# Kernel optimization log

Measured on AMD Instinct MI355X. Metric: run time of the kernel, lower is better.

The kernel has to match this reference:

```python
import jax, jax.numpy as jnp
import numpy as np

B, T, I, H = 64, 512, 1024, 1024

def setup_inputs() -> dict:
    key = jax.random.key(0)
    k1, k2, k3, k4, k5 = jax.random.split(key, 5)
    s_x = 1.0 / np.sqrt(I)
    s_h = 1.0 / np.sqrt(H)
    return {
        "x": jax.random.normal(k1, (B, T, I), dtype=jnp.float32),
        "Wx": jax.random.uniform(k2, (I, H), minval=-s_x, maxval=s_x, dtype=jnp.float32),
        "bx": jax.random.uniform(k3, (H,), minval=-s_x, maxval=s_x, dtype=jnp.float32),
        "Wh": jax.random.uniform(k4, (H, H), minval=-s_h, maxval=s_h, dtype=jnp.float32),
        "bh": jax.random.uniform(k5, (H,), minval=-s_h, maxval=s_h, dtype=jnp.float32),
    }

def reference(x, Wx, bx, Wh, bh):
    # Precompute input projections for all timesteps in one big GEMM: [B,T,H]
    xproj = jnp.einsum("bti,ih->bth", x, Wx) + bx + bh
    h0 = jnp.zeros((x.shape[0], Wh.shape[0]), dtype=x.dtype)

    def step(h, xp_t):
        h_new = jnp.tanh(xp_t + h @ Wh)
        return h_new, h_new

    # scan over time: xproj transposed to [T,B,H]
    h_last, outs = jax.lax.scan(step, h0, jnp.swapaxes(xproj, 0, 1))
    return jnp.swapaxes(outs, 0, 1), h_last
```

## Files before the change

kernel.cpp:

```cpp
#include <hip/hip_runtime.h>


#define Bdim 64
#define Tdim 512
#define Idim 1024
#define Hdim 1024
#define Mdim (Bdim * Tdim)

typedef __attribute__((ext_vector_type(8))) short bf16x8;
typedef __attribute__((ext_vector_type(4))) float f32x4;
typedef __attribute__((ext_vector_type(4))) unsigned int u32x4;

__device__ __forceinline__ float tanh_fast(float x) {
  float e = __expf(2.0f * x);
  return 1.0f - 2.0f / (e + 1.0f);
}
__device__ __forceinline__ unsigned int f2bf(float f) {
  unsigned int u = __float_as_uint(f);
  return (u + 0x7FFFu + ((u >> 16) & 1u)) >> 16;
}
__device__ __forceinline__ unsigned int pack2(float lo, float hi) {
  return f2bf(lo) | (f2bf(hi) << 16);
}

__global__ __launch_bounds__(256) void cvt_transpose(
    const float* __restrict__ src, unsigned short* __restrict__ dst) {
  __shared__ float t[32][33];
  const int bx = blockIdx.x * 32;
  const int by = blockIdx.y * 32;
  const int ty = threadIdx.x >> 3;
  const int tx = threadIdx.x & 7;
  float4 v = *(const float4*)&src[(size_t)(by + ty) * 1024 + bx + tx * 4];
  t[ty][tx * 4 + 0] = v.x; t[ty][tx * 4 + 1] = v.y;
  t[ty][tx * 4 + 2] = v.z; t[ty][tx * 4 + 3] = v.w;
  __syncthreads();
  ushort4 o;
  o.x = (unsigned short)f2bf(t[tx * 4 + 0][ty]);
  o.y = (unsigned short)f2bf(t[tx * 4 + 1][ty]);
  o.z = (unsigned short)f2bf(t[tx * 4 + 2][ty]);
  o.w = (unsigned short)f2bf(t[tx * 4 + 3][ty]);
  *(ushort4*)&dst[(size_t)(bx + ty) * 1024 + by + tx * 4] = o;
}

__global__ __launch_bounds__(256) void xg_mfma(
    const float* __restrict__ X,
    const unsigned short* __restrict__ WxT,
    const float* __restrict__ bx, const float* __restrict__ bh,
    float* __restrict__ C) {
  __shared__ char sAB[16384] __attribute__((aligned(16)));
  char* sA = sAB;
  char* sB = sAB + 8192;
  const int tid = threadIdx.x;
  const int m0 = blockIdx.y * 128;
  const int n0 = blockIdx.x * 128;
  const int w = tid >> 6, l = tid & 63;
  const int wm = (w >> 1) * 64, wn = (w & 1) * 64;
  const int r2 = tid >> 1, kh = tid & 1;

  f32x4 acc[4][4];
#pragma unroll
  for (int i = 0; i < 4; ++i)
#pragma unroll
    for (int j = 0; j < 4; ++j) acc[i][j] = (f32x4){0.f, 0.f, 0.f, 0.f};

  for (int k0 = 0; k0 < Idim; k0 += 32) {
    const float* xa = &X[(size_t)(m0 + r2) * Idim + k0 + kh * 16];
    float4 a0 = *(const float4*)(xa + 0), a1 = *(const float4*)(xa + 4);
    float4 a2 = *(const float4*)(xa + 8), a3 = *(const float4*)(xa + 12);
    const char* wb = (const char*)&WxT[(size_t)(n0 + r2) * Idim + k0 + kh * 16];
    u32x4 b0 = *(const u32x4*)wb;
    u32x4 b1 = *(const u32x4*)(wb + 16);
    __syncthreads();
    u32x4 pa0 = {pack2(a0.x, a0.y), pack2(a0.z, a0.w),
                 pack2(a1.x, a1.y), pack2(a1.z, a1.w)};
    u32x4 pa1 = {pack2(a2.x, a2.y), pack2(a2.z, a2.w),
                 pack2(a3.x, a3.y), pack2(a3.z, a3.w)};
    const int sw = (r2 & 7) << 4;
    const int rb = r2 * 64 + kh * 32;
    *(u32x4*)(sA + ((rb + 0) ^ sw)) = pa0;
    *(u32x4*)(sA + ((rb + 16) ^ sw)) = pa1;
    *(u32x4*)(sB + ((rb + 0) ^ sw)) = b0;
    *(u32x4*)(sB + ((rb + 16) ^ sw)) = b1;
    __syncthreads();
    bf16x8 af[4], bf[4];
#pragma unroll
    for (int i = 0; i < 4; ++i) {
      int ra = wm + i * 16 + (l & 15);
      af[i] = *(const bf16x8*)(sA + ((ra * 64 + (l >> 4) * 16) ^ ((ra & 7) << 4)));
      int rn = wn + i * 16 + (l & 15);
      bf[i] = *(const bf16x8*)(sB + ((rn * 64 + (l >> 4) * 16) ^ ((rn & 7) << 4)));
    }
#pragma unroll
    for (int i = 0; i < 4; ++i)
#pragma unroll
      for (int j = 0; j < 4; ++j)
        acc[i][j] = __builtin_amdgcn_mfma_f32_16x16x32_bf16(af[i], bf[j],
                                                            acc[i][j], 0, 0, 0);
  }
  float bias[4];
#pragma unroll
  for (int j = 0; j < 4; ++j) {
    int c = n0 + wn + j * 16 + (l & 15);
    bias[j] = bx[c] + bh[c];
  }
#pragma unroll
  for (int i = 0; i < 4; ++i) {
    int rbase = m0 + wm + i * 16 + (l >> 4) * 4;
#pragma unroll
    for (int j = 0; j < 4; ++j) {
      int c = n0 + wn + j * 16 + (l & 15);
#pragma unroll
      for (int r = 0; r < 4; ++r)
        C[(size_t)(rbase + r) * Hdim + c] = acc[i][j][r] + bias[j];
    }
  }
}

__global__ __launch_bounds__(512, 2) void rnn_scan(
    const unsigned short* __restrict__ WhT,
    float* __restrict__ out,
    float* __restrict__ hlast,
    unsigned long long* hbuf) {
  const int bid = blockIdx.x;
  const int cl = bid & 3;
  const int cg = bid >> 2;
  const int tid = threadIdx.x;
  const int w = tid >> 6;
  const int l = tid & 63;
  const int n0 = cg * 64;

  __shared__ char smem[32768 + 33280] __attribute__((aligned(16)));
  char* smh = smem;
  char* smp = smem + 32768;

  bf16x8 bfrag[16];
  {
    const int col = n0 + (l & 15);
    const int kb = (w << 7) + ((l >> 4) << 3);
#pragma unroll
    for (int nt = 0; nt < 4; ++nt)
#pragma unroll
      for (int kt = 0; kt < 4; ++kt)
        bfrag[nt * 4 + kt] =
            *(const bf16x8*)&WhT[(size_t)(col + nt * 16) * 1024 + kb + kt * 32];
  }

  const int fb = tid >> 5;
  const int jj = tid & 31;
  const int c0 = 2 * jj;
  const int b_abs = cl * 16 + fb;
  const int nt0 = c0 >> 4;
  const int lane0 = ((fb >> 2) << 4) | (c0 & 15);
  const int reg4 = (fb & 3) * 4;
  const size_t obase = ((size_t)b_abs * Tdim) * Hdim + n0 + c0;

  float2 xp = *(const float2*)&out[obase];

  for (int t = 0; t < Tdim; ++t) {
    float sum0 = 0.f, sum1 = 0.f;
    if (t > 0) {
      const int arow = l & 15;
      const int ab = arow * 2048 + (w << 8) + ((l >> 4) << 4);
      const int sw = (arow & 7) << 4;
      bf16x8 af[4];
#pragma unroll
      for (int kt = 0; kt < 4; ++kt)
        af[kt] = *(const bf16x8*)(smh + ((ab + kt * 64) ^ sw));
#pragma unroll
      for (int nt = 0; nt < 4; ++nt) {
        f32x4 a = {0.f, 0.f, 0.f, 0.f};
#pragma unroll
        for (int kt = 0; kt < 4; ++kt)
          a = __builtin_amdgcn_mfma_f32_16x16x32_bf16(af[kt], bfrag[nt * 4 + kt],
                                                      a, 0, 0, 0);
        *(f32x4*)(smp + (((w * 4 + nt) * 65 + l) << 4)) = a;
      }
      __syncthreads();
#pragma unroll
      for (int w8 = 0; w8 < 8; ++w8) {
        const char* p0 = smp + (((w8 * 4 + nt0) * 65 + lane0) << 4) + reg4;
        sum0 += *(const float*)p0;
        sum1 += *(const float*)(p0 + 16);
      }
    }
    float h0 = tanh_fast(xp.x + sum0);
    float h1 = tanh_fast(xp.y + sum1);
    if (t == Tdim - 1) {
      *(float2*)&out[obase + (size_t)t * Hdim] = make_float2(h0, h1);
      *(float2*)&hlast[(size_t)b_abs * Hdim + n0 + c0] = make_float2(h0, h1);
      break;
    }
    const int par = (t + 1) & 1;
    unsigned long long pv =
        ((unsigned long long)(unsigned int)(t + 1) << 32) |
        (unsigned long long)pack2(h0, h1);
    __hip_atomic_store(&hbuf[(size_t)par * 32768 + (size_t)b_abs * 512 +
                             (n0 >> 1) + jj],
                       pv, __ATOMIC_RELAXED, __HIP_MEMORY_SCOPE_AGENT);
    *(float2*)&out[obase + (size_t)t * Hdim] = make_float2(h0, h1);
    xp = *(const float2*)&out[obase + (size_t)(t + 1) * Hdim];
    {
      const char* src =
          (const char*)hbuf + (size_t)par * 262144 + (size_t)cl * 65536;
      u32x4 v[8];
      const unsigned int tgt = (unsigned int)(t + 1);
      for (;;) {
#pragma unroll
        for (int i = 0; i < 8; ++i) {
          const char* p = src + ((size_t)(tid + i * 512) << 4);
          asm volatile("global_load_dwordx4 %0, %1, off sc0 sc1"
                       : "=v"(v[i]) : "v"(p) : "memory");
        }
        asm volatile("s_waitcnt vmcnt(0)" ::: "memory");
        bool ok = true;
#pragma unroll
        for (int i = 0; i < 8; ++i)
          ok = ok && (v[i].y >= tgt) && (v[i].w >= tgt);
        if (ok) break;
        __builtin_amdgcn_s_sleep(1);
      }
      __builtin_amdgcn_sched_barrier(0);
#pragma unroll
      for (int i = 0; i < 8; ++i) {
        int chunk = tid + i * 512;
        int bl = chunk >> 8;
        int cp0 = (chunk << 1) & 511;
        int byte = (bl * 2048 + cp0 * 4) ^ ((bl & 7) << 4);
        *(uint2*)(smh + byte) = make_uint2(v[i].x, v[i].z);
      }
    }
    __syncthreads();
  }
}

extern "C" void kernel_launch(void* const* d_in, const int* in_sizes, int n_in,
                              void* d_out, int out_size, void* d_ws,
                              size_t ws_size, hipStream_t stream) {
  const float* x  = (const float*)d_in[0];
  const float* Wx = (const float*)d_in[1];
  const float* bx = (const float*)d_in[2];
  const float* Wh = (const float*)d_in[3];
  const float* bh = (const float*)d_in[4];
  float* out = (float*)d_out;
  float* hlast = out + (size_t)Bdim * Tdim * Hdim;
  unsigned long long* hbuf = (unsigned long long*)d_ws;
  unsigned short* WxT = (unsigned short*)((char*)d_ws + 524288);
  unsigned short* WhT = (unsigned short*)((char*)d_ws + 524288 + 2097152);

  hipMemsetAsync(d_ws, 0, 524288, stream);

  dim3 gt(32, 32);
  cvt_transpose<<<gt, dim3(256), 0, stream>>>(Wx, WxT);
  cvt_transpose<<<gt, dim3(256), 0, stream>>>(Wh, WhT);
  xg_mfma<<<dim3(Hdim / 128, Mdim / 128), dim3(256), 0, stream>>>(x, WxT, bx,
                                                                  bh, out);
  rnn_scan<<<dim3(64), dim3(512), 0, stream>>>(WhT, out, hlast, hbuf);
}
```

Baseline: 1.824 ms.

## Replace per-element timestamped h exchange with per-block flags and narrower batch partition

The recurrent scan now splits work as 8 batch clusters of 8 rows by 8 column groups of 128, so each block holds twice as many Wh fragments and only gathers 8 batch rows of h per step. Before, every thread polled 64-bit values that each carried a step tag. Now each block writes plain 32-bit packed bf16 h values, barriers, and raises one per-block flag. A single wave polls the 8 flags of its cluster with a ballot, then all threads load the h slice once. This is meant to cut cross-block polling traffic and the bytes exchanged per step, at the cost of more register pressure and extra barriers, with correctness relying on the vmcnt wait ordering the h stores before the flag store.

```diff
diff --git a/kernel.cpp b/kernel.cpp
--- a/kernel.cpp
+++ b/kernel.cpp
@@ -100,87 +100,98 @@
   float bias[4];
 #pragma unroll
   for (int j = 0; j < 4; ++j) {
-    int c = n0 + wn + j * 16 + (l & 15);
-    bias[j] = bx[c] + bh[c];
+    int cc = n0 + wn + j * 16 + (l & 15);
+    bias[j] = bx[cc] + bh[cc];
   }
 #pragma unroll
   for (int i = 0; i < 4; ++i) {
     int rbase = m0 + wm + i * 16 + (l >> 4) * 4;
 #pragma unroll
     for (int j = 0; j < 4; ++j) {
-      int c = n0 + wn + j * 16 + (l & 15);
+      int cc = n0 + wn + j * 16 + (l & 15);
 #pragma unroll
       for (int r = 0; r < 4; ++r)
-        C[(size_t)(rbase + r) * Hdim + c] = acc[i][j][r] + bias[j];
-    }
-  }
+        C[(size_t)(rbase + r) * Hdim + cc] = acc[i][j][r] + bias[j];
+    }
+  }
+}
+
+__global__ void clear_flags(unsigned int* flags) {
+  __hip_atomic_store(&flags[threadIdx.x], 0u, __ATOMIC_RELAXED,
+                     __HIP_MEMORY_SCOPE_AGENT);
 }
 
 __global__ __launch_bounds__(512, 2) void rnn_scan(
     const unsigned short* __restrict__ WhT,
     float* __restrict__ out,
     float* __restrict__ hlast,
-    unsigned long long* hbuf) {
+    unsigned int* hbuf,
+    unsigned int* flags) {
   const int bid = blockIdx.x;
-  const int cl = bid & 3;
-  const int cg = bid >> 2;
+  const int c = bid & 7;
+  const int m = bid >> 3;
   const int tid = threadIdx.x;
   const int w = tid >> 6;
   const int l = tid & 63;
-  const int n0 = cg * 64;
-
-  __shared__ char smem[32768 + 33280] __attribute__((aligned(16)));
+  const int n0 = m * 128;
+
+  __shared__ char smem[16384 + 66560] __attribute__((aligned(16)));
   char* smh = smem;
-  char* smp = smem + 32768;
-
-  bf16x8 bfrag[16];
+  char* smp = smem + 16384;
+
+  bf16x8 bfrag[32];
   {
+    const int kb = (w << 7) + ((l >> 4) << 3);
     const int col = n0 + (l & 15);
-    const int kb = (w << 7) + ((l >> 4) << 3);
-#pragma unroll
-    for (int nt = 0; nt < 4; ++nt)
+#pragma unroll
+    for (int nt = 0; nt < 8; ++nt)
 #pragma unroll
       for (int kt = 0; kt < 4; ++kt)
         bfrag[nt * 4 + kt] =
             *(const bf16x8*)&WhT[(size_t)(col + nt * 16) * 1024 + kb + kt * 32];
   }
 
-  const int fb = tid >> 5;
-  const int jj = tid & 31;
-  const int c0 = 2 * jj;
-  const int b_abs = cl * 16 + fb;
+  const int fb = tid >> 6;
+  const int cpl = tid & 63;
+  const int c0 = cpl * 2;
+  const int b_abs = c * 8 + fb;
   const int nt0 = c0 >> 4;
   const int lane0 = ((fb >> 2) << 4) | (c0 & 15);
-  const int reg4 = (fb & 3) * 4;
-  const size_t obase = ((size_t)b_abs * Tdim) * Hdim + n0 + c0;
+  const int regb = (fb & 3) * 4;
+  const size_t obase = (size_t)b_abs * ((size_t)Tdim * Hdim) + n0 + c0;
+  unsigned int* pub = &hbuf[(size_t)b_abs * 512 + m * 64 + cpl];
+  unsigned int* myflag = &flags[c * 32 + m];
+  const unsigned int* pollf = &flags[c * 32 + (l & 7)];
 
   float2 xp = *(const float2*)&out[obase];
 
   for (int t = 0; t < Tdim; ++t) {
     float sum0 = 0.f, sum1 = 0.f;
     if (t > 0) {
-      const int arow = l & 15;
-      const int ab = arow * 2048 + (w << 8) + ((l >> 4) << 4);
-      const int sw = (arow & 7) << 4;
+      const int arow = l & 7;
+      const int abase = arow * 2048 + (w << 8) + ((l >> 4) << 4);
+      const int sw = arow << 4;
       bf16x8 af[4];
 #pragma unroll
       for (int kt = 0; kt < 4; ++kt)
-        af[kt] = *(const bf16x8*)(smh + ((ab + kt * 64) ^ sw));
-#pragma unroll
-      for (int nt = 0; nt < 4; ++nt) {
+        af[kt] = *(const bf16x8*)(smh + ((abase + kt * 64) ^ sw));
+#pragma unroll
+      for (int nt = 0; nt < 8; ++nt) {
         f32x4 a = {0.f, 0.f, 0.f, 0.f};
 #pragma unroll
         for (int kt = 0; kt < 4; ++kt)
           a = __builtin_amdgcn_mfma_f32_16x16x32_bf16(af[kt], bfrag[nt * 4 + kt],
                                                       a, 0, 0, 0);
-        *(f32x4*)(smp + (((w * 4 + nt) * 65 + l) << 4)) = a;
+        *(f32x4*)(smp + (((w * 8 + nt) * 65 + l) << 4)) = a;
       }
-      __syncthreads();
+      asm volatile("s_waitcnt lgkmcnt(0)" ::: "memory");
+      __builtin_amdgcn_s_barrier();
+      asm volatile("" ::: "memory");
 #pragma unroll
       for (int w8 = 0; w8 < 8; ++w8) {
-        const char* p0 = smp + (((w8 * 4 + nt0) * 65 + lane0) << 4) + reg4;
-        sum0 += *(const float*)p0;
-        sum1 += *(const float*)(p0 + 16);
+        const char* p = smp + (((w8 * 8 + nt0) * 65 + lane0) << 4) + regb;
+        sum0 += *(const float*)p;
+        sum1 += *(const float*)(p + 16);
       }
     }
     float h0 = tanh_fast(xp.x + sum0);
@@ -191,45 +202,50 @@
       break;
     }
     const int par = (t + 1) & 1;
-    unsigned long long pv =
-        ((unsigned long long)(unsigned int)(t + 1) << 32) |
-        (unsigned long long)pack2(h0, h1);
-    __hip_atomic_store(&hbuf[(size_t)par * 32768 + (size_t)b_abs * 512 +
-                             (n0 >> 1) + jj],
-                       pv, __ATOMIC_RELAXED, __HIP_MEMORY_SCOPE_AGENT);
+    __hip_atomic_store(pub + par * 32768, pack2(h0, h1), __ATOMIC_RELAXED,
+                       __HIP_MEMORY_SCOPE_AGENT);
+    asm volatile("" ::: "memory");
     *(float2*)&out[obase + (size_t)t * Hdim] = make_float2(h0, h1);
     xp = *(const float2*)&out[obase + (size_t)(t + 1) * Hdim];
-    {
-      const char* src =
-          (const char*)hbuf + (size_t)par * 262144 + (size_t)cl * 65536;
-      u32x4 v[8];
+    asm volatile("s_waitcnt vmcnt(2)" ::: "memory");
+    __builtin_amdgcn_s_barrier();
+    asm volatile("" ::: "memory");
+    if (tid == 0)
+      __hip_atomic_store(myflag, (unsigned int)(t + 1), __ATOMIC_RELAXED,
+                         __HIP_MEMORY_SCOPE_AGENT);
+    if (w == 7) {
       const unsigned int tgt = (unsigned int)(t + 1);
       for (;;) {
-#pragma unroll
-        for (int i = 0; i < 8; ++i) {
-          const char* p = src + ((size_t)(tid + i * 512) << 4);
-          asm volatile("global_load_dwordx4 %0, %1, off sc0 sc1"
-                       : "=v"(v[i]) : "v"(p) : "memory");
-        }
-        asm volatile("s_waitcnt vmcnt(0)" ::: "memory");
-        bool ok = true;
-#pragma unroll
-        for (int i = 0; i < 8; ++i)
-          ok = ok && (v[i].y >= tgt) && (v[i].w >= tgt);
-        if (ok) break;
-        __builtin_amdgcn_s_sleep(1);
+        unsigned int v;
+        asm volatile(
+            "global_load_dword %0, %1, off sc0 sc1\n\ts_waitcnt vmcnt(0)"
+            : "=v"(v) : "v"(pollf) : "memory");
+        if (__ballot(v >= tgt) == ~0ull) break;
+        __builtin_amdgcn_s_sleep(2);
       }
+    }
+    asm volatile("" ::: "memory");
+    __builtin_amdgcn_s_barrier();
+    asm volatile("" ::: "memory");
+    {
+      const char* src = (const char*)hbuf + (size_t)par * 131072 +
+                        (size_t)(c * 8 + (tid >> 6)) * 2048 + (tid & 63) * 32;
+      u32x4 d0, d1;
+      asm volatile(
+          "global_load_dwordx4 %0, %2, off sc0 sc1\n\t"
+          "global_load_dwordx4 %1, %2, off offset:16 sc0 sc1\n\t"
+          "s_waitcnt vmcnt(0)"
+          : "=&v"(d0), "=&v"(d1) : "v"(src) : "memory");
       __builtin_amdgcn_sched_barrier(0);
-#pragma unroll
-      for (int i = 0; i < 8; ++i) {
-        int chunk = tid + i * 512;
-        int bl = chunk >> 8;
-        int cp0 = (chunk << 1) & 511;
-        int byte = (bl * 2048 + cp0 * 4) ^ ((bl & 7) << 4);
-        *(uint2*)(smh + byte) = make_uint2(v[i].x, v[i].z);
-      }
-    }
-    __syncthreads();
+      const int r = tid >> 6;
+      const int base = r * 2048 + (tid & 63) * 32;
+      const int sw = r << 4;
+      *(u32x4*)(smh + (base ^ sw)) = d0;
+      *(u32x4*)(smh + ((base + 16) ^ sw)) = d1;
+    }
+    asm volatile("s_waitcnt lgkmcnt(0)" ::: "memory");
+    __builtin_amdgcn_s_barrier();
+    asm volatile("" ::: "memory");
   }
 }
 
@@ -243,16 +259,16 @@
   const float* bh = (const float*)d_in[4];
   float* out = (float*)d_out;
   float* hlast = out + (size_t)Bdim * Tdim * Hdim;
-  unsigned long long* hbuf = (unsigned long long*)d_ws;
-  unsigned short* WxT = (unsigned short*)((char*)d_ws + 524288);
-  unsigned short* WhT = (unsigned short*)((char*)d_ws + 524288 + 2097152);
-
-  hipMemsetAsync(d_ws, 0, 524288, stream);
-
+  unsigned int* flags = (unsigned int*)d_ws;
+  unsigned int* hbuf = (unsigned int*)((char*)d_ws + 4096);
+  unsigned short* WxT = (unsigned short*)((char*)d_ws + 4096 + 262144);
+  unsigned short* WhT = (unsigned short*)((char*)d_ws + 4096 + 262144 + 2097152);
+
+  clear_flags<<<1, dim3(256), 0, stream>>>(flags);
   dim3 gt(32, 32);
   cvt_transpose<<<gt, dim3(256), 0, stream>>>(Wx, WxT);
   cvt_transpose<<<gt, dim3(256), 0, stream>>>(Wh, WhT);
   xg_mfma<<<dim3(Hdim / 128, Mdim / 128), dim3(256), 0, stream>>>(x, WxT, bx,
                                                                   bh, out);
-  rnn_scan<<<dim3(64), dim3(512), 0, stream>>>(WhT, out, hlast, hbuf);
-}
+  rnn_scan<<<dim3(64), dim3(512), 0, stream>>>(WhT, out, hlast, hbuf, flags);
+}
```

New measurement: 1.546 ms. 1.18x faster.
